# Kernel tuning notes

Hardware: AMD Instinct MI355X
Metric: run time of the kernel (lower is better)

The kernel has to match this reference:

```python
import jax, jax.numpy as jnp
import numpy as np

T = 200000


def _sine_layer(tvec, A, w, phi, phic, wc):
    # tvec: (t,), A/w/phi: (n,1), phic/wc: (1,)
    phi_static = jax.nn.relu(phic)  # (1,)
    w_static = jax.nn.relu(wc)
    ph = jax.nn.relu(phi) + phi_static  # (n,1)
    ww = jax.nn.relu(w) + w_static
    sine = A * jnp.sin(ww * tvec[None, :] + ph)  # (n,t)
    return sine, phi_static, w_static


def _selector_layer(tvec, wave_input, w, phi, phic, wc, phi_prev, w_prev):
    # wave_input: (n,t), w/phi: (m,n), phic/wc/phi_prev/w_prev: (1,)
    # NOTE: phi_prev/w_prev passed but phi_prev flag is False in the network,
    # so they are NOT added (matches torch: `if self.phi_prev and ...`).
    phi_static = jax.nn.relu(phic)
    w_static = jax.nn.relu(wc)
    ph = (jax.nn.relu(phi) + phi_static)[:, :, None]  # (m,n,1)
    ww = (jax.nn.relu(w) + w_static)[:, :, None]
    sine = 0.5 * jnp.sin(ww * tvec[None, None, :] + ph) + 0.5  # (m,n,t)
    out = jnp.einsum('mnt,nt->mt', sine, wave_input)  # (m,t)
    return out, phi_static, w_static


def setup_inputs() -> dict:
    key = jax.random.key(0)
    ks = jax.random.split(key, 18)
    r = lambda k, s: jax.random.normal(k, s, dtype=jnp.float32)
    return {
        'initial_wave_input': r(ks[0], (20, T)),
        'A0': r(ks[1], (20, 1)), 'w0': r(ks[2], (20, 1)), 'phi0': r(ks[3], (20, 1)),
        'wc0': r(ks[4], (1,)), 'phic0': r(ks[5], (1,)),
        'w1': r(ks[6], (25, 20)), 'phi1': r(ks[7], (25, 20)),
        'wc1': r(ks[8], (1,)), 'phic1': r(ks[9], (1,)),
        'w2': r(ks[10], (30, 25)), 'phi2': r(ks[11], (30, 25)),
        'wc2': r(ks[12], (1,)), 'phic2': r(ks[13], (1,)),
        'w3': r(ks[14], (1, 30)), 'phi3': r(ks[15], (1, 30)),
        'wc3': r(ks[16], (1,)), 'phic3': r(ks[17], (1,)),
    }


def reference(initial_wave_input, A0, w0, phi0, wc0, phic0,
              w1, phi1, wc1, phic1, w2, phi2, wc2, phic2,
              w3, phi3, wc3, phic3):
    tvec = jnp.linspace(1.0, 1000.0, T, dtype=jnp.float32)
    # initial_wave_input is an argument of the torch module but is never used.
    s, phi, w = _sine_layer(tvec, A0, w0, phi0, phic0, wc0)
    s, phi, w = _selector_layer(tvec, s, w1, phi1, phic1, wc1, phi, w)
    s, phi, w = _selector_layer(tvec, s, w2, phi2, phic2, wc2, phi, w)
    s, phi, w = _selector_layer(tvec, s, w3, phi3, phic3, wc3, phi, w)
    return s  # (1, t)
```

## Files before the change

### kernel.cpp

```cpp
#include <hip/hip_runtime.h>
#include <hip/hip_bf16.h>

#define T_TOTAL 200000
#define INV2PI 0.15915494309189535f

__device__ float g_P[2620];

__device__ __forceinline__ float relu_f(float x) { return fmaxf(x, 0.0f); }

__device__ __forceinline__ float sin_rev(float rev) {
    return __builtin_amdgcn_sinf(__builtin_amdgcn_fractf(rev));
}

__global__ void prep_kernel(
    const float* __restrict__ A0,
    const float* __restrict__ w0, const float* __restrict__ phi0,
    const float* __restrict__ wc0, const float* __restrict__ phic0,
    const float* __restrict__ w1, const float* __restrict__ phi1,
    const float* __restrict__ wc1, const float* __restrict__ phic1,
    const float* __restrict__ w2, const float* __restrict__ phi2,
    const float* __restrict__ wc2, const float* __restrict__ phic2,
    const float* __restrict__ w3, const float* __restrict__ phi3,
    const float* __restrict__ wc3, const float* __restrict__ phic3)
{
    const int tid = blockIdx.x * blockDim.x + threadIdx.x;
    const int stride = blockDim.x * gridDim.x;

    const float ws0 = relu_f(wc0[0]), ps0 = relu_f(phic0[0]);
    const float ws1 = relu_f(wc1[0]), ps1 = relu_f(phic1[0]);
    const float ws2 = relu_f(wc2[0]), ps2 = relu_f(phic2[0]);
    const float ws3 = relu_f(wc3[0]), ps3 = relu_f(phic3[0]);

    for (int n = tid; n < 20; n += stride) {
        g_P[2 * n]     = (relu_f(w0[n])   + ws0) * INV2PI;
        g_P[2 * n + 1] = (relu_f(phi0[n]) + ps0) * INV2PI;
        g_P[40 + n]    = A0[n];
    }
    for (int k = tid; k < 500; k += stride) {
        const int m = k / 20, n = k % 20;
        const int d = 60 + 2 * (n * 25 + m);
        g_P[d]     = (relu_f(w1[k])   + ws1) * INV2PI;
        g_P[d + 1] = (relu_f(phi1[k]) + ps1) * INV2PI;
    }
    for (int k = tid; k < 750; k += stride) {
        const int m = k / 25, n = k % 25;
        const int d = 1060 + 2 * (n * 30 + m);
        g_P[d]     = (relu_f(w2[k])   + ws2) * INV2PI;
        g_P[d + 1] = (relu_f(phi2[k]) + ps2) * INV2PI;
    }
    for (int k = tid; k < 30; k += stride) {
        g_P[2560 + 2 * k]     = (relu_f(w3[k])   + ws3) * INV2PI;
        g_P[2560 + 2 * k + 1] = (relu_f(phi3[k]) + ps3) * INV2PI;
    }
}

__launch_bounds__(256)
__global__ void wave_main(float* __restrict__ out)
{
    __shared__ float sh[25 * 256];

    const int tid = threadIdx.x;
    const int t = blockIdx.x * 256 + tid;
    const float tv = fmaf((float)t, 999.0f / 199999.0f, 1.0f);

    float sum0 = 0.0f;
#pragma unroll
    for (int n = 0; n < 20; ++n) {
        float rev = fmaf(g_P[2 * n], tv, g_P[2 * n + 1]);
        float v = g_P[40 + n] * sin_rev(rev);
        sh[n * 256 + tid] = v;
        sum0 += v;
    }

    float acc1[25];
#pragma unroll
    for (int m = 0; m < 25; ++m) acc1[m] = 0.0f;
    __syncthreads();
#pragma clang loop unroll(disable)
    for (int n = 0; n < 20; ++n) {
        const float s0n = sh[n * 256 + tid];
        const float* __restrict__ p = &g_P[60 + 50 * n];
#pragma unroll
        for (int m = 0; m < 25; ++m) {
            float rev = fmaf(p[2 * m], tv, p[2 * m + 1]);
            acc1[m] = fmaf(sin_rev(rev), s0n, acc1[m]);
        }
    }
    __syncthreads();
    float sum1 = 0.0f;
#pragma unroll
    for (int m = 0; m < 25; ++m) {
        float v = fmaf(0.5f, acc1[m], 0.5f * sum0);
        sh[m * 256 + tid] = v;
        sum1 += v;
    }

    float acc2[30];
#pragma unroll
    for (int m = 0; m < 30; ++m) acc2[m] = 0.0f;
    __syncthreads();
#pragma clang loop unroll(disable)
    for (int n = 0; n < 25; ++n) {
        const float s1n = sh[n * 256 + tid];
        const float* __restrict__ p = &g_P[1060 + 60 * n];
#pragma unroll
        for (int m = 0; m < 30; ++m) {
            float rev = fmaf(p[2 * m], tv, p[2 * m + 1]);
            acc2[m] = fmaf(sin_rev(rev), s1n, acc2[m]);
        }
    }
    float sum2 = 0.0f;
    float s2v[30];
#pragma unroll
    for (int m = 0; m < 30; ++m) {
        s2v[m] = fmaf(0.5f, acc2[m], 0.5f * sum1);
        sum2 += s2v[m];
    }

    float acc3 = 0.0f;
#pragma unroll
    for (int n = 0; n < 30; ++n) {
        float rev = fmaf(g_P[2560 + 2 * n], tv, g_P[2560 + 2 * n + 1]);
        acc3 = fmaf(sin_rev(rev), s2v[n], acc3);
    }
    if (t < T_TOTAL)
        out[t] = fmaf(0.5f, acc3, 0.5f * sum2);
}

extern "C" void kernel_launch(void* const* d_in, const int* in_sizes, int n_in,
                              void* d_out, int out_size, void* d_ws, size_t ws_size,
                              hipStream_t stream) {
    (void)in_sizes; (void)n_in; (void)d_ws; (void)ws_size;
    const float* A0    = (const float*)d_in[1];
    const float* w0    = (const float*)d_in[2];
    const float* phi0  = (const float*)d_in[3];
    const float* wc0   = (const float*)d_in[4];
    const float* phic0 = (const float*)d_in[5];
    const float* w1    = (const float*)d_in[6];
    const float* phi1  = (const float*)d_in[7];
    const float* wc1   = (const float*)d_in[8];
    const float* phic1 = (const float*)d_in[9];
    const float* w2    = (const float*)d_in[10];
    const float* phi2  = (const float*)d_in[11];
    const float* wc2   = (const float*)d_in[12];
    const float* phic2 = (const float*)d_in[13];
    const float* w3    = (const float*)d_in[14];
    const float* phi3  = (const float*)d_in[15];
    const float* wc3   = (const float*)d_in[16];
    const float* phic3 = (const float*)d_in[17];

    float* out = (float*)d_out;

    hipLaunchKernelGGL(prep_kernel, dim3(11), dim3(256), 0, stream,
                       A0, w0, phi0, wc0, phic0,
                       w1, phi1, wc1, phic1,
                       w2, phi2, wc2, phic2,
                       w3, phi3, wc3, phic3);

    const int grid = (T_TOTAL + 255) / 256;
    hipLaunchKernelGGL(wave_main, dim3(grid), dim3(256), 0, stream, out);
}
```

Baseline: 64.12 us.

## Split each timestep's output neurons across four waves per block

Each block now handles 64 timesteps, and its four wavefronts divide the output neurons of each layer between them (5, 7 and 8 per wave). Per-layer activations are exchanged through shared memory with barriers in between. The parameter table is padded to 28 and 32 columns so the wave-uniform slices line up, and the padding is zeroed. This cuts per-thread register arrays (acc1 drops from 25 to 7 entries, acc2 from 30 to 8), which should raise occupancy and quadruple the block count. The cost is extra barriers and leaving three waves idle in the final layer. The tail bounds check is removed because 200000 divides evenly by 64.

```diff
diff --git a/kernel.cpp b/kernel.cpp
--- a/kernel.cpp
+++ b/kernel.cpp
@@ -4,7 +4,7 @@
 #define T_TOTAL 200000
 #define INV2PI 0.15915494309189535f
 
-__device__ float g_P[2620];
+__device__ float g_P[2840];
 
 __device__ __forceinline__ float relu_f(float x) { return fmaxf(x, 0.0f); }
 
@@ -36,101 +36,119 @@
         g_P[2 * n + 1] = (relu_f(phi0[n]) + ps0) * INV2PI;
         g_P[40 + n]    = A0[n];
     }
-    for (int k = tid; k < 500; k += stride) {
-        const int m = k / 20, n = k % 20;
-        const int d = 60 + 2 * (n * 25 + m);
-        g_P[d]     = (relu_f(w1[k])   + ws1) * INV2PI;
-        g_P[d + 1] = (relu_f(phi1[k]) + ps1) * INV2PI;
+    for (int k = tid; k < 20 * 28; k += stride) {
+        const int n = k / 28, m = k % 28;
+        const int d = 60 + 2 * k;
+        if (m < 25) {
+            const int s = m * 20 + n;
+            g_P[d]     = (relu_f(w1[s])   + ws1) * INV2PI;
+            g_P[d + 1] = (relu_f(phi1[s]) + ps1) * INV2PI;
+        } else {
+            g_P[d] = 0.0f; g_P[d + 1] = 0.0f;
+        }
     }
-    for (int k = tid; k < 750; k += stride) {
-        const int m = k / 25, n = k % 25;
-        const int d = 1060 + 2 * (n * 30 + m);
-        g_P[d]     = (relu_f(w2[k])   + ws2) * INV2PI;
-        g_P[d + 1] = (relu_f(phi2[k]) + ps2) * INV2PI;
+    for (int k = tid; k < 25 * 32; k += stride) {
+        const int n = k / 32, m = k % 32;
+        const int d = 1180 + 2 * k;
+        if (m < 30) {
+            const int s = m * 25 + n;
+            g_P[d]     = (relu_f(w2[s])   + ws2) * INV2PI;
+            g_P[d + 1] = (relu_f(phi2[s]) + ps2) * INV2PI;
+        } else {
+            g_P[d] = 0.0f; g_P[d + 1] = 0.0f;
+        }
     }
     for (int k = tid; k < 30; k += stride) {
-        g_P[2560 + 2 * k]     = (relu_f(w3[k])   + ws3) * INV2PI;
-        g_P[2560 + 2 * k + 1] = (relu_f(phi3[k]) + ps3) * INV2PI;
+        g_P[2780 + 2 * k]     = (relu_f(w3[k])   + ws3) * INV2PI;
+        g_P[2780 + 2 * k + 1] = (relu_f(phi3[k]) + ps3) * INV2PI;
     }
 }
 
 __launch_bounds__(256)
 __global__ void wave_main(float* __restrict__ out)
 {
-    __shared__ float sh[25 * 256];
+    __shared__ float sh0[20 * 64];
+    __shared__ float sh1[25 * 64];
+    __shared__ float sh2[30 * 64];
 
     const int tid = threadIdx.x;
-    const int t = blockIdx.x * 256 + tid;
+    const int l = tid & 63;
+    const int w = __builtin_amdgcn_readfirstlane(tid >> 6);
+    const int t = blockIdx.x * 64 + l;
     const float tv = fmaf((float)t, 999.0f / 199999.0f, 1.0f);
 
-    float sum0 = 0.0f;
+    {
+        const float* __restrict__ p = &g_P[10 * w];
+        const float* __restrict__ a = &g_P[40 + 5 * w];
 #pragma unroll
-    for (int n = 0; n < 20; ++n) {
-        float rev = fmaf(g_P[2 * n], tv, g_P[2 * n + 1]);
-        float v = g_P[40 + n] * sin_rev(rev);
-        sh[n * 256 + tid] = v;
-        sum0 += v;
-    }
-
-    float acc1[25];
-#pragma unroll
-    for (int m = 0; m < 25; ++m) acc1[m] = 0.0f;
-    __syncthreads();
-#pragma clang loop unroll(disable)
-    for (int n = 0; n < 20; ++n) {
-        const float s0n = sh[n * 256 + tid];
-        const float* __restrict__ p = &g_P[60 + 50 * n];
-#pragma unroll
-        for (int m = 0; m < 25; ++m) {
-            float rev = fmaf(p[2 * m], tv, p[2 * m + 1]);
-            acc1[m] = fmaf(sin_rev(rev), s0n, acc1[m]);
+        for (int i = 0; i < 5; ++i) {
+            float rev = fmaf(p[2 * i], tv, p[2 * i + 1]);
+            sh0[(5 * w + i) * 64 + l] = a[i] * sin_rev(rev);
         }
     }
     __syncthreads();
+
+    float acc1[7];
+#pragma unroll
+    for (int j = 0; j < 7; ++j) acc1[j] = 0.0f;
+    float sum0 = 0.0f;
+#pragma clang loop unroll(disable)
+    for (int n = 0; n < 20; ++n) {
+        const float s0n = sh0[n * 64 + l];
+        sum0 += s0n;
+        const float* __restrict__ p = &g_P[60 + 56 * n + 14 * w];
+#pragma unroll
+        for (int j = 0; j < 7; ++j) {
+            float rev = fmaf(p[2 * j], tv, p[2 * j + 1]);
+            acc1[j] = fmaf(sin_rev(rev), s0n, acc1[j]);
+        }
+    }
+#pragma unroll
+    for (int j = 0; j < 7; ++j) {
+        const int m = 7 * w + j;
+        if (m < 25) sh1[m * 64 + l] = fmaf(0.5f, acc1[j], 0.5f * sum0);
+    }
+    __syncthreads();
+
+    float acc2[8];
+#pragma unroll
+    for (int j = 0; j < 8; ++j) acc2[j] = 0.0f;
     float sum1 = 0.0f;
-#pragma unroll
-    for (int m = 0; m < 25; ++m) {
-        float v = fmaf(0.5f, acc1[m], 0.5f * sum0);
-        sh[m * 256 + tid] = v;
-        sum1 += v;
-    }
-
-    float acc2[30];
-#pragma unroll
-    for (int m = 0; m < 30; ++m) acc2[m] = 0.0f;
-    __syncthreads();
 #pragma clang loop unroll(disable)
     for (int n = 0; n < 25; ++n) {
-        const float s1n = sh[n * 256 + tid];
-        const float* __restrict__ p = &g_P[1060 + 60 * n];
+        const float s1n = sh1[n * 64 + l];
+        sum1 += s1n;
+        const float* __restrict__ p = &g_P[1180 + 64 * n + 16 * w];
 #pragma unroll
-        for (int m = 0; m < 30; ++m) {
-            float rev = fmaf(p[2 * m], tv, p[2 * m + 1]);
-            acc2[m] = fmaf(sin_rev(rev), s1n, acc2[m]);
+        for (int j = 0; j < 8; ++j) {
+            float rev = fmaf(p[2 * j], tv, p[2 * j + 1]);
+            acc2[j] = fmaf(sin_rev(rev), s1n, acc2[j]);
         }
     }
-    float sum2 = 0.0f;
-    float s2v[30];
 #pragma unroll
-    for (int m = 0; m < 30; ++m) {
-        s2v[m] = fmaf(0.5f, acc2[m], 0.5f * sum1);
-        sum2 += s2v[m];
+    for (int j = 0; j < 8; ++j) {
+        const int m = 8 * w + j;
+        if (m < 30) sh2[m * 64 + l] = fmaf(0.5f, acc2[j], 0.5f * sum1);
     }
+    __syncthreads();
 
-    float acc3 = 0.0f;
+    if (w == 0) {
+        float acc3 = 0.0f, sum2 = 0.0f;
 #pragma unroll
-    for (int n = 0; n < 30; ++n) {
-        float rev = fmaf(g_P[2560 + 2 * n], tv, g_P[2560 + 2 * n + 1]);
-        acc3 = fmaf(sin_rev(rev), s2v[n], acc3);
+        for (int n = 0; n < 30; ++n) {
+            const float s2n = sh2[n * 64 + l];
+            sum2 += s2n;
+            float rev = fmaf(g_P[2780 + 2 * n], tv, g_P[2780 + 2 * n + 1]);
+            acc3 = fmaf(sin_rev(rev), s2n, acc3);
+        }
+        out[t] = fmaf(0.5f, acc3, 0.5f * sum2);
     }
-    if (t < T_TOTAL)
-        out[t] = fmaf(0.5f, acc3, 0.5f * sum2);
 }
 
 extern "C" void kernel_launch(void* const* d_in, const int* in_sizes, int n_in,
                               void* d_out, int out_size, void* d_ws, size_t ws_size,
                               hipStream_t stream) {
-    (void)in_sizes; (void)n_in; (void)d_ws; (void)ws_size;
+    (void)in_sizes; (void)n_in; (void)d_ws; (void)ws_size; (void)out_size;
     const float* A0    = (const float*)d_in[1];
     const float* w0    = (const float*)d_in[2];
     const float* phi0  = (const float*)d_in[3];
@@ -157,6 +175,6 @@
                        w2, phi2, wc2, phic2,
                        w3, phi3, wc3, phic3);
 
-    const int grid = (T_TOTAL + 255) / 256;
+    const int grid = T_TOTAL / 64;
     hipLaunchKernelGGL(wave_main, dim3(grid), dim3(256), 0, stream, out);
 }
```

After: 53.51 us. 16.5% less time.
